# Kernel tuning notes

Measured on AMD Instinct MI355X. Metric: run time of the kernel, lower is better.

## Reference

```python
import jax, jax.numpy as jnp
import numpy as np

EPS = 1e-6      # eps used in token2map / map2token weight normalization
LN_EPS = 1e-5   # torch nn.LayerNorm default


def layernorm(x, w, b):
    m = jnp.mean(x, axis=-1, keepdims=True)
    xc = x - m
    v = jnp.mean(xc * xc, axis=-1, keepdims=True)
    return xc * jax.lax.rsqrt(v + LN_EPS) * w + b


def grid_index(H_init, W_init, H, W):
    # nearest-neighbor map: flattened feature-map index for each init-grid cell
    r = (jnp.arange(H_init) * H) // H_init
    c = (jnp.arange(W_init) * W) // W_init
    return (r[:, None] * W + c[None, :]).reshape(-1)  # [N_init]


def token2map(x, idx_token, H, W, H_init, W_init):
    # tokens [B,N,C] -> feature map [B,H,W,C] via weighted scatter-mean
    B, N, C = x.shape
    idx_hw = grid_index(H_init, W_init, H, W)                    # [N_init]
    counts = jnp.zeros((H * W,), x.dtype).at[idx_hw].add(1.0)    # identical across batch
    w = (1.0 / (counts + EPS))[idx_hw]                           # [N_init]
    src = jnp.take_along_axis(x, idx_token[..., None], axis=1)   # [B,N_init,C]
    out = jnp.zeros((B, H * W, C), x.dtype).at[:, idx_hw, :].add(src * w[None, :, None])
    return out.reshape(B, H, W, C)


def map2token(fmap, idx_token, N, H_init, W_init):
    # feature map [B,H,W,C] -> tokens [B,N,C]: mean of member grid cells per token
    B, H, W, C = fmap.shape
    idx_hw = grid_index(H_init, W_init, H, W)
    bidx = jnp.arange(B)[:, None]
    counts = jnp.zeros((B, N), fmap.dtype).at[bidx, idx_token].add(1.0)
    wt = jnp.take_along_axis(1.0 / (counts + EPS), idx_token, axis=1)  # [B,N_init]
    src = fmap.reshape(B, H * W, C)[:, idx_hw, :]                      # [B,N_init,C]
    return jnp.zeros((B, N, C), fmap.dtype).at[bidx, idx_token].add(src * wt[..., None])


def _forward(x, token_score, idx_token,
             norm1_w, norm1_b, q_w, q_b, kv_w, kv_b, sr_w, sr_b, srn_w, srn_b,
             proj_w, proj_b, norm2_w, norm2_b, fc1_w, fc1_b, skip_w, dw_w, dw_b,
             fc2_w, fc2_b, H, W, H_init, W_init, token_num, num_heads):
    B, N, C = x.shape
    d = C // num_heads
    scale = d ** -0.5
    sr = 2  # sr_ratio

    xn = layernorm(x, norm1_w, norm1_b)  # q_dict['x'] = norm1(x); kv_dict is q_dict

    # ---- TCFormerDynamicAttention ----
    q = (xn @ q_w + q_b).reshape(B, N, num_heads, d).transpose(0, 2, 1, 3)  # [B,h,N,d]
    tmp = jnp.concatenate([xn, token_score], axis=-1)            # [B,N,C+1]
    tmp_map = token2map(tmp, idx_token, H, W, H_init, W_init)    # [B,H,W,C+1]
    kv_map, conf_map = tmp_map[..., :C], tmp_map[..., C]
    kv = jax.lax.conv_general_dilated(kv_map, sr_w, (sr, sr), 'VALID',
        dimension_numbers=('NHWC', 'HWIO', 'NHWC')) + sr_b       # sr conv, stride 2
    M = (H // sr) * (W // sr)
    kv = layernorm(kv.reshape(B, M, C), srn_w, srn_b)
    conf = conf_map.reshape(B, H // sr, sr, W // sr, sr).mean(axis=(2, 4)).reshape(B, M)

    kv = (kv @ kv_w + kv_b).reshape(B, M, 2, num_heads, d)
    k = kv[:, :, 0].transpose(0, 2, 1, 3)                        # [B,h,M,d]
    v = kv[:, :, 1].transpose(0, 2, 1, 3)
    attn = jnp.einsum('bhnd,bhmd->bhnm', q * scale, k) + conf[:, None, None, :]
    attn = jax.nn.softmax(attn, axis=-1)
    a = jnp.einsum('bhnm,bhmd->bhnd', attn, v).transpose(0, 2, 1, 3).reshape(B, N, C)
    x = x + (a @ proj_w + proj_b)

    # ---- TCMLP ----
    h = layernorm(x, norm2_w, norm2_b) @ fc1_w + fc1_b           # [B,N,H1]
    hmap = token2map(h, idx_token, H, W, H_init, W_init)         # [B,H,W,H1]
    hmap = jax.lax.conv_general_dilated(hmap, dw_w, (1, 1), ((1, 1), (1, 1)),
        dimension_numbers=('NHWC', 'HWIO', 'NHWC'),
        feature_group_count=h.shape[-1]) + dw_b                  # depthwise 3x3
    hc = h * skip_w + map2token(hmap, idx_token, N, H_init, W_init)  # skip = dw 1x1 conv1d
    hc = jax.nn.gelu(hc, approximate=False)
    return x + (hc @ fc2_w + fc2_b)


def setup_inputs() -> dict:
    B, N, C, H1 = 8, 1568, 256, 1024
    H = W = 56
    H_init = W_init = 112
    key = jax.random.key(0)
    ks = jax.random.split(key, 16)
    r = lambda i, shape, s=0.02: jax.random.normal(ks[i], shape, jnp.float32) * s
    return {
        'x': jax.random.normal(ks[0], (B, N, C), jnp.float32),
        'token_score': jax.random.normal(ks[1], (B, N, 1), jnp.float32),
        'idx_token': jax.random.randint(ks[2], (B, H_init * W_init), 0, N),
        'norm1_w': jnp.ones((C,), jnp.float32), 'norm1_b': jnp.zeros((C,), jnp.float32),
        'q_w': r(3, (C, C)), 'q_b': jnp.zeros((C,), jnp.float32),
        'kv_w': r(4, (C, 2 * C)), 'kv_b': jnp.zeros((2 * C,), jnp.float32),
        'sr_w': r(5, (2, 2, C, C)), 'sr_b': jnp.zeros((C,), jnp.float32),
        'srn_w': jnp.ones((C,), jnp.float32), 'srn_b': jnp.zeros((C,), jnp.float32),
        'proj_w': r(6, (C, C)), 'proj_b': jnp.zeros((C,), jnp.float32),
        'norm2_w': jnp.ones((C,), jnp.float32), 'norm2_b': jnp.zeros((C,), jnp.float32),
        'fc1_w': r(7, (C, H1)), 'fc1_b': jnp.zeros((H1,), jnp.float32),
        'skip_w': 1.0 + r(8, (H1,), 0.1),
        'dw_w': r(9, (3, 3, 1, H1), 0.1), 'dw_b': jnp.zeros((H1,), jnp.float32),
        'fc2_w': r(10, (H1, C)), 'fc2_b': jnp.zeros((C,), jnp.float32),
        'H': H, 'W': W, 'H_init': H_init, 'W_init': W_init,
        'token_num': N, 'num_heads': 8,
    }


def reference(x, token_score, idx_token, norm1_w, norm1_b, q_w, q_b, kv_w, kv_b,
              sr_w, sr_b, srn_w, srn_b, proj_w, proj_b, norm2_w, norm2_b,
              fc1_w, fc1_b, skip_w, dw_w, dw_b, fc2_w, fc2_b,
              H, W, H_init, W_init, token_num, num_heads):
    return _forward(x, token_score, idx_token, norm1_w, norm1_b, q_w, q_b, kv_w, kv_b,
                    sr_w, sr_b, srn_w, srn_b, proj_w, proj_b, norm2_w, norm2_b,
                    fc1_w, fc1_b, skip_w, dw_w, dw_b, fc2_w, fc2_b,
                    H, W, H_init, W_init, token_num, num_heads)
```

## Files before the change

### kernel.cpp

```cpp
#include <hip/hip_runtime.h>
#include <math.h>

#define BB 8
#define NTOK 1568
#define CD 256
#define HIMG 56
#define WIMG 56
#define HWSZ 3136
#define HIG 112
#define WIG 112
#define NI 12544
#define MKV 784
#define MPAD 800
#define NHEADS 8
#define HEADD 32
#define HH1 1024
#define ROWS1 (BB*NTOK)
#define ROWSK (BB*MKV)
#define LOG2E 1.4426950408889634f

typedef unsigned short bfu;
typedef __attribute__((ext_vector_type(4))) unsigned short bf4;
typedef __attribute__((ext_vector_type(8))) unsigned short bf8;
typedef __attribute__((ext_vector_type(8))) short s8v;
typedef __attribute__((ext_vector_type(4))) float f4v;
typedef __attribute__((ext_vector_type(16))) float f16v;

__device__ inline float b2f(bfu u) { union { unsigned i; float f; } x; x.i = (unsigned)u << 16; return x.f; }
__device__ inline bfu f2b(float f) {
  union { float f; unsigned i; } x; x.f = f;
  unsigned r = x.i + 0x7fffu + ((x.i >> 16) & 1u);
  return (bfu)(r >> 16);
}
__device__ inline int get_isb(const unsigned* probe) { return probe[0] == 0x3F803F80u ? 1 : 0; }
__device__ inline float ldd(const void* p, size_t i, int isb) {
  return isb ? b2f(((const bfu*)p)[i]) : ((const float*)p)[i];
}
__device__ inline int xswz(int wg, int nwg) {
  return (nwg & 7) ? wg : (wg & 7) * (nwg >> 3) + (wg >> 3);
}

__global__ __launch_bounds__(256) void wtr_tile(const void* __restrict__ w0,
                                                const void* __restrict__ w1,
                                                const void* __restrict__ w2,
                                                const void* __restrict__ w3,
                                                const void* __restrict__ w4,
                                                const void* __restrict__ w5,
                                                const void* __restrict__ w6,
                                                const void* __restrict__ w7,
                                                bfu* __restrict__ wtb,
                                                const unsigned* __restrict__ probe) {
  int isb = get_isb(probe);
  int bid = blockIdx.x, tid = threadIdx.x;
  if (bid >= 1024) {
    int idx = (bid - 1024) * 256 + tid;
    if (idx < 9216) wtb[1048576 + idx] = f2b(ldd(w6, idx, isb));
    else            wtb[1048576 + idx] = f2b(ldd(w7, idx - 9216, isb));
    return;
  }
  const void* W; int K, N; bfu* Wt; int tloc;
  if (bid < 64)       { W = w0; K = 256;  N = 256;  Wt = wtb;          tloc = bid; }
  else if (bid < 320) { W = w1; K = 1024; N = 256;  Wt = wtb + 65536;  tloc = bid - 64; }
  else if (bid < 448) { W = w2; K = 256;  N = 512;  Wt = wtb + 327680; tloc = bid - 320; }
  else if (bid < 512) { W = w3; K = 256;  N = 256;  Wt = wtb + 458752; tloc = bid - 448; }
  else if (bid < 768) { W = w4; K = 256;  N = 1024; Wt = wtb + 524288; tloc = bid - 512; }
  else                { W = w5; K = 1024; N = 256;  Wt = wtb + 786432; tloc = bid - 768; }
  int ntn = N >> 5;
  int tn = tloc % ntn, tk = tloc / ntn;
  int n0 = tn * 32, k0 = tk * 32;
  __shared__ float s[32][33];
  int tx = tid & 31, ty = tid >> 5;
#pragma unroll
  for (int i = 0; i < 4; i++) {
    int k = ty + 8 * i;
    s[k][tx] = ldd(W, (size_t)(k0 + k) * N + n0 + tx, isb);
  }
  __syncthreads();
#pragma unroll
  for (int i = 0; i < 4; i++) {
    int n = ty + 8 * i;
    Wt[(size_t)(n0 + n) * K + k0 + tx] = f2b(s[tx][n]);
  }
}

__global__ __launch_bounds__(256) void ln_kernel(const void* __restrict__ in, int inmode,
                                                 const void* __restrict__ w,
                                                 const void* __restrict__ bta,
                                                 bfu* __restrict__ out,
                                                 const unsigned* __restrict__ probe) {
  int isb = get_isb(probe);
  int im = (inmode == 2) ? isb : inmode;
  int blk = xswz(blockIdx.x, gridDim.x);
  int wv = threadIdx.x >> 6, lane = threadIdx.x & 63;
  int row = blk * 4 + wv;
  int c4 = lane * 4;
  float v[4];
  if (im) {
    bf4 t = *(const bf4*)((const bfu*)in + (size_t)row * CD + c4);
#pragma unroll
    for (int j = 0; j < 4; j++) v[j] = b2f(t[j]);
  } else {
    float4 t = *(const float4*)((const float*)in + (size_t)row * CD + c4);
    v[0] = t.x; v[1] = t.y; v[2] = t.z; v[3] = t.w;
  }
  float s1 = v[0] + v[1] + v[2] + v[3];
  float s2 = v[0] * v[0] + v[1] * v[1] + v[2] * v[2] + v[3] * v[3];
#pragma unroll
  for (int off = 1; off < 64; off <<= 1) {
    s1 += __shfl_xor(s1, off);
    s2 += __shfl_xor(s2, off);
  }
  float m = s1 * (1.0f / CD);
  float inv = rsqrtf(s2 * (1.0f / CD) - m * m + 1e-5f);
  bf4 ov;
#pragma unroll
  for (int j = 0; j < 4; j++)
    ov[j] = f2b((v[j] - m) * inv * ldd(w, c4 + j, isb) + ldd(bta, c4 + j, isb));
  *(bf4*)(out + (size_t)row * CD + c4) = ov;
}

__global__ __launch_bounds__(256) void gemm2ph(const bfu* __restrict__ A,
                                               const bfu* __restrict__ Bt,
                                               const void* __restrict__ bias,
                                               const void* __restrict__ resid, int rmode,
                                               void* __restrict__ Cc, int cmode,
                                               void* __restrict__ aux,
                                               int K, int Ncols,
                                               const unsigned* __restrict__ probe) {
  int isb = get_isb(probe);
  int rm = (rmode == 1) ? (isb ? 3 : 2) : rmode;
  int cm = (cmode == 2) ? (isb ? 0 : 1) : cmode;
  __shared__ bfu As[2][64][40];
  __shared__ bfu Bs[2][64][40];
  int t = threadIdx.x;
  int nbx = Ncols >> 6;
  int id = xswz(blockIdx.x, gridDim.x);
  int row0 = (id / nbx) * 64, col0 = (id % nbx) * 64;
  int sr = t >> 2, sc = (t & 3) * 8;
  int w = t >> 6, lane = t & 63;
  int li = lane & 15, q = lane >> 4;
  int wm = w * 16;
  const bfu* pa = A + (size_t)(row0 + sr) * K + sc;
  const bfu* pb = Bt + (size_t)(col0 + sr) * K + sc;
  f4v zz = {0.f, 0.f, 0.f, 0.f};
  f4v acc[4];
#pragma unroll
  for (int ni = 0; ni < 4; ni++) acc[ni] = zz;
  s8v la = *(const s8v*)(pa);
  s8v lb = *(const s8v*)(pb);
  int cur = 0;
  for (int k0 = 32; k0 <= K; k0 += 32) {
    *(s8v*)(&As[cur][sr][sc]) = la;
    *(s8v*)(&Bs[cur][sr][sc]) = lb;
    __syncthreads();
    if (k0 < K) {
      la = *(const s8v*)(pa + k0);
      lb = *(const s8v*)(pb + k0);
    }
    s8v af  = *(const s8v*)(&As[cur][wm + li][q * 8]);
    s8v bf0 = *(const s8v*)(&Bs[cur][li][q * 8]);
    s8v bf1 = *(const s8v*)(&Bs[cur][16 + li][q * 8]);
    s8v bf2 = *(const s8v*)(&Bs[cur][32 + li][q * 8]);
    s8v bf3 = *(const s8v*)(&Bs[cur][48 + li][q * 8]);
    __builtin_amdgcn_s_setprio(1);
    acc[0] = __builtin_amdgcn_mfma_f32_16x16x32_bf16(af, bf0, acc[0], 0, 0, 0);
    acc[1] = __builtin_amdgcn_mfma_f32_16x16x32_bf16(af, bf1, acc[1], 0, 0, 0);
    acc[2] = __builtin_amdgcn_mfma_f32_16x16x32_bf16(af, bf2, acc[2], 0, 0, 0);
    acc[3] = __builtin_amdgcn_mfma_f32_16x16x32_bf16(af, bf3, acc[3], 0, 0, 0);
    __builtin_amdgcn_s_setprio(0);
    cur ^= 1;
  }
  float bw[4];
#pragma unroll
  for (int ni = 0; ni < 4; ni++) bw[ni] = ldd(bias, col0 + ni * 16 + li, isb);
#pragma unroll
  for (int ni = 0; ni < 4; ni++) {
    int col = col0 + ni * 16 + li;
#pragma unroll
    for (int r = 0; r < 4; r++) {
      int row = row0 + wm + q * 4 + r;
      size_t base = (size_t)row * Ncols + col;
      float v = acc[ni][r] + bw[ni];
      if (rm == 2) v += ((const float*)resid)[base];
      else if (rm == 3) v += b2f(((const bfu*)resid)[base]);
      if (cm == 0) ((bfu*)Cc)[base] = f2b(v);
      else if (cm == 1) ((float*)Cc)[base] = v;
      else {
        if (col < 256) ((bfu*)Cc)[base] = f2b(v);
        else {
          int bb = row / MKV, mm = row - bb * MKV;
          ((bfu*)aux)[((size_t)(bb * 256) + (col - 256)) * MPAD + mm] = f2b(v);
        }
      }
    }
  }
}

__global__ __launch_bounds__(256) void akv_kernel(const bfu* __restrict__ xn,
                                                  const void* __restrict__ tscore,
                                                  const int* __restrict__ idx_token,
                                                  bfu* __restrict__ Akv,
                                                  float* __restrict__ conf,
                                                  const unsigned* __restrict__ probe) {
  int isb = get_isb(probe);
  int blk = xswz(blockIdx.x, gridDim.x), tid = threadIdx.x;
  int b = blk / MKV, m = blk % MKV;
  int i2 = m / 28, j2 = m % 28;
  __shared__ int nn[16];
  __shared__ float cacc[16];
  if (tid < 16) {
    int a = (tid >> 3) & 1, kb = (tid >> 2) & 1, di = (tid >> 1) & 1, dj = tid & 1;
    int ti = 4 * i2 + 2 * a + di, tj = 4 * j2 + 2 * kb + dj;
    int n = idx_token[b * NI + ti * WIG + tj];
    nn[tid] = n;
    cacc[tid] = ldd(tscore, b * NTOK + n, isb);
  }
  __syncthreads();
  const float w4 = 1.0f / (4.0f + 1e-6f);
  int g = tid >> 6, c4 = (tid & 63) * 4;
  bf4 a0 = *(const bf4*)(xn + (size_t)(b * NTOK + nn[g * 4 + 0]) * CD + c4);
  bf4 a1 = *(const bf4*)(xn + (size_t)(b * NTOK + nn[g * 4 + 1]) * CD + c4);
  bf4 a2 = *(const bf4*)(xn + (size_t)(b * NTOK + nn[g * 4 + 2]) * CD + c4);
  bf4 a3 = *(const bf4*)(xn + (size_t)(b * NTOK + nn[g * 4 + 3]) * CD + c4);
  bf4 rv;
#pragma unroll
  for (int j = 0; j < 4; j++)
    rv[j] = f2b(w4 * (b2f(a0[j]) + b2f(a1[j]) + b2f(a2[j]) + b2f(a3[j])));
  *(bf4*)(Akv + (size_t)blk * 1024 + g * CD + c4) = rv;
  if (tid == 0) {
    float s = 0.f;
    for (int k = 0; k < 16; k++) s += cacc[k];
    conf[b * MPAD + m] = 0.25f * w4 * s * 5.656854249492381f;
  }
}

__global__ __launch_bounds__(256) void pad_kernel(bfu* __restrict__ vt, float* __restrict__ conf) {
  int t = blockIdx.x * 256 + threadIdx.x;
  int b = t / 4096, rem = t % 4096;
  int d = rem / 16, m = MKV + (rem % 16);
  vt[((size_t)(b * 256 + d)) * MPAD + m] = 0;
  if (t < 128) conf[(t / 16) * MPAD + MKV + (t % 16)] = -1e30f;
}

__global__ __launch_bounds__(256) void attn_kernel(const bfu* __restrict__ qb,
                                                   const bfu* __restrict__ kv,
                                                   const bfu* __restrict__ vt,
                                                   const float* __restrict__ conf,
                                                   bfu* __restrict__ out) {
  __shared__ float sdata[4][64][34];
  int tid = threadIdx.x;
  int w = tid >> 6, lane = tid & 63;
  int l31 = lane & 31, hi = lane >> 5;
  int blk = xswz(blockIdx.x, gridDim.x);
  int qt = blk % 25, tt = blk / 25;
  int hh = tt & 7, b = tt >> 3;
  int n0 = qt * 64;
  int two = (qt < 24);
  const bfu* qrow1 = qb + (size_t)(b * NTOK + n0 + l31) * CD + hh * HEADD + hi * 8;
  s8v qfA1 = *(const s8v*)(qrow1);
  s8v qfB1 = *(const s8v*)(qrow1 + 16);
  s8v qfA2 = {0, 0, 0, 0, 0, 0, 0, 0}, qfB2 = qfA2;
  if (two) {
    const bfu* qrow2 = qrow1 + (size_t)32 * CD;
    qfA2 = *(const s8v*)(qrow2);
    qfB2 = *(const s8v*)(qrow2 + 16);
  }
  const float scale = 0.17677669529663689f * LOG2E;
  const bfu* kbase = kv + hh * HEADD + hi * 8;
  const bfu* vbase = vt + ((size_t)(b * 256 + hh * HEADD + l31)) * MPAD + hi * 8;
  const float* cbase = conf + b * MPAD + 4 * hi;
  f16v oc1, oc2;
#pragma unroll
  for (int r = 0; r < 16; r++) { oc1[r] = 0.f; oc2[r] = 0.f; }
  float lr1 = 0.f, lr2 = 0.f;
  int w32 = w * 32;
  const bfu* kp0 = kbase + (size_t)(b * MKV + w32 + l31) * 512;
  s8v kfA = *(const s8v*)(kp0);
  s8v kfB = *(const s8v*)(kp0 + 16);
  s8v vfA = *(const s8v*)(vbase + w32);
  s8v vfB = *(const s8v*)(vbase + w32 + 16);
  float4 cf0 = *(const float4*)(cbase + w32);
  float4 cf1 = *(const float4*)(cbase + w32 + 8);
  float4 cf2 = *(const float4*)(cbase + w32 + 16);
  float4 cf3 = *(const float4*)(cbase + w32 + 24);
  for (int m0 = w32; m0 < MPAD; m0 += 128) {
    s8v ckA = kfA, ckB = kfB, cvA = vfA, cvB = vfB;
    float4 d0 = cf0, d1 = cf1, d2 = cf2, d3 = cf3;
    int m1 = m0 + 128;
    if (m1 < MPAD) {
      int mA = m1 + l31; if (mA > MKV - 1) mA = MKV - 1;
      const bfu* kp = kbase + (size_t)(b * MKV + mA) * 512;
      kfA = *(const s8v*)(kp);
      kfB = *(const s8v*)(kp + 16);
      vfA = *(const s8v*)(vbase + m1);
      vfB = *(const s8v*)(vbase + m1 + 16);
      cf0 = *(const float4*)(cbase + m1);
      cf1 = *(const float4*)(cbase + m1 + 8);
      cf2 = *(const float4*)(cbase + m1 + 16);
      cf3 = *(const float4*)(cbase + m1 + 24);
    }
    f16v cseed;
    cseed[0] = d0.x; cseed[1] = d0.y; cseed[2] = d0.z; cseed[3] = d0.w;
    cseed[4] = d1.x; cseed[5] = d1.y; cseed[6] = d1.z; cseed[7] = d1.w;
    cseed[8] = d2.x; cseed[9] = d2.y; cseed[10] = d2.z; cseed[11] = d2.w;
    cseed[12] = d3.x; cseed[13] = d3.y; cseed[14] = d3.z; cseed[15] = d3.w;
    __builtin_amdgcn_s_setprio(1);
    f16v c = __builtin_amdgcn_mfma_f32_32x32x16_bf16(ckA, qfA1, cseed, 0, 0, 0);
    c = __builtin_amdgcn_mfma_f32_32x32x16_bf16(ckB, qfB1, c, 0, 0, 0);
    __builtin_amdgcn_s_setprio(0);
    {
      float p[16], ps0 = 0.f, ps1 = 0.f, ps2 = 0.f, ps3 = 0.f;
#pragma unroll
      for (int r = 0; r < 16; r++) {
        p[r] = __builtin_amdgcn_exp2f(c[r] * scale);
        if ((r & 3) == 0) ps0 += p[r];
        else if ((r & 3) == 1) ps1 += p[r];
        else if ((r & 3) == 2) ps2 += p[r];
        else ps3 += p[r];
      }
      lr1 += (ps0 + ps1) + (ps2 + ps3);
      unsigned Z[8];
#pragma unroll
      for (int a2 = 0; a2 < 8; a2++)
        asm("v_cvt_pk_bf16_f32 %0, %1, %2" : "=v"(Z[a2]) : "v"(p[2 * a2]), "v"(p[2 * a2 + 1]));
      asm("v_permlane32_swap_b32 %0, %1" : "+v"(Z[0]), "+v"(Z[2]));
      asm("v_permlane32_swap_b32 %0, %1" : "+v"(Z[1]), "+v"(Z[3]));
      asm("v_permlane32_swap_b32 %0, %1" : "+v"(Z[4]), "+v"(Z[6]));
      asm("v_permlane32_swap_b32 %0, %1" : "+v"(Z[5]), "+v"(Z[7]));
      union { unsigned u[4]; s8v v; } B1, B2;
      B1.u[0] = Z[0]; B1.u[1] = Z[1]; B1.u[2] = Z[2]; B1.u[3] = Z[3];
      B2.u[0] = Z[4]; B2.u[1] = Z[5]; B2.u[2] = Z[6]; B2.u[3] = Z[7];
      __builtin_amdgcn_s_setprio(1);
      oc1 = __builtin_amdgcn_mfma_f32_32x32x16_bf16(cvA, B1.v, oc1, 0, 0, 0);
      oc1 = __builtin_amdgcn_mfma_f32_32x32x16_bf16(cvB, B2.v, oc1, 0, 0, 0);
      __builtin_amdgcn_s_setprio(0);
    }
    if (two) {
      __builtin_amdgcn_s_setprio(1);
      f16v c2 = __builtin_amdgcn_mfma_f32_32x32x16_bf16(ckA, qfA2, cseed, 0, 0, 0);
      c2 = __builtin_amdgcn_mfma_f32_32x32x16_bf16(ckB, qfB2, c2, 0, 0, 0);
      __builtin_amdgcn_s_setprio(0);
      float p[16], ps0 = 0.f, ps1 = 0.f, ps2 = 0.f, ps3 = 0.f;
#pragma unroll
      for (int r = 0; r < 16; r++) {
        p[r] = __builtin_amdgcn_exp2f(c2[r] * scale);
        if ((r & 3) == 0) ps0 += p[r];
        else if ((r & 3) == 1) ps1 += p[r];
        else if ((r & 3) == 2) ps2 += p[r];
        else ps3 += p[r];
      }
      lr2 += (ps0 + ps1) + (ps2 + ps3);
      unsigned Z[8];
#pragma unroll
      for (int a2 = 0; a2 < 8; a2++)
        asm("v_cvt_pk_bf16_f32 %0, %1, %2" : "=v"(Z[a2]) : "v"(p[2 * a2]), "v"(p[2 * a2 + 1]));
      asm("v_permlane32_swap_b32 %0, %1" : "+v"(Z[0]), "+v"(Z[2]));
      asm("v_permlane32_swap_b32 %0, %1" : "+v"(Z[1]), "+v"(Z[3]));
      asm("v_permlane32_swap_b32 %0, %1" : "+v"(Z[4]), "+v"(Z[6]));
      asm("v_permlane32_swap_b32 %0, %1" : "+v"(Z[5]), "+v"(Z[7]));
      union { unsigned u[4]; s8v v; } B1, B2;
      B1.u[0] = Z[0]; B1.u[1] = Z[1]; B1.u[2] = Z[2]; B1.u[3] = Z[3];
      B2.u[0] = Z[4]; B2.u[1] = Z[5]; B2.u[2] = Z[6]; B2.u[3] = Z[7];
      __builtin_amdgcn_s_setprio(1);
      oc2 = __builtin_amdgcn_mfma_f32_32x32x16_bf16(cvA, B1.v, oc2, 0, 0, 0);
      oc2 = __builtin_amdgcn_mfma_f32_32x32x16_bf16(cvB, B2.v, oc2, 0, 0, 0);
      __builtin_amdgcn_s_setprio(0);
    }
  }
#pragma unroll
  for (int r = 0; r < 16; r++) { sdata[w][lane][r] = oc1[r]; sdata[w][lane][17 + r] = oc2[r]; }
  sdata[w][lane][16] = lr1;
  sdata[w][lane][33] = lr2;
  __syncthreads();
  if (w == 0 || (w == 1 && two)) {
    int base = w * 17;
    float s[17];
#pragma unroll
    for (int r = 0; r < 17; r++)
      s[r] = sdata[0][lane][base + r] + sdata[1][lane][base + r] +
             sdata[2][lane][base + r] + sdata[3][lane][base + r];
    float l = s[16];
    l += __shfl_xor(l, 32);
    float inv = 1.0f / l;
    bfu* op = out + (size_t)(b * NTOK + n0 + w * 32 + l31) * CD + hh * HEADD + 4 * hi;
#pragma unroll
    for (int g = 0; g < 4; g++) {
      bf4 o;
#pragma unroll
      for (int u = 0; u < 4; u++) o[u] = f2b(s[4 * g + u] * inv);
      *(bf4*)(op + 8 * g) = o;
    }
  }
}

__global__ __launch_bounds__(128) void hmap_kernel(const bfu* __restrict__ h,
                                                   const int* __restrict__ idx_token,
                                                   bfu* __restrict__ hmap) {
  int blk = xswz(blockIdx.x, gridDim.x), tid = threadIdx.x;
  int b = blk / HWSZ, cell = blk % HWSZ;
  int i = cell / WIMG, j = cell % WIMG;
  __shared__ int nn[4];
  if (tid < 4) {
    int di = tid >> 1, dj = tid & 1;
    nn[tid] = idx_token[b * NI + (2 * i + di) * WIG + (2 * j + dj)];
  }
  __syncthreads();
  const float w4 = 1.0f / (4.0f + 1e-6f);
  int c8 = tid * 8;
  bf8 a0 = *(const bf8*)(h + (size_t)(b * NTOK + nn[0]) * HH1 + c8);
  bf8 a1 = *(const bf8*)(h + (size_t)(b * NTOK + nn[1]) * HH1 + c8);
  bf8 a2 = *(const bf8*)(h + (size_t)(b * NTOK + nn[2]) * HH1 + c8);
  bf8 a3 = *(const bf8*)(h + (size_t)(b * NTOK + nn[3]) * HH1 + c8);
  bf8 rv;
#pragma unroll
  for (int j2 = 0; j2 < 8; j2++)
    rv[j2] = f2b(w4 * (b2f(a0[j2]) + b2f(a1[j2]) + b2f(a2[j2]) + b2f(a3[j2])));
  *(bf8*)(hmap + (size_t)blk * HH1 + c8) = rv;
}

__global__ __launch_bounds__(256) void dw_kernel(const bfu* __restrict__ hmap,
                                                 const bfu* __restrict__ dwt,
                                                 const bfu* __restrict__ dbt,
                                                 bfu* __restrict__ dwout) {
  int blk = xswz(blockIdx.x, gridDim.x);
  int j4 = blk % 14; int rem = blk / 14;
  int i = rem % HIMG; int b = rem / HIMG;
  int tid = threadIdx.x;
  int c4 = tid * 4;
  int j0 = j4 * 4;
  float wf[9][4];
#pragma unroll
  for (int k = 0; k < 9; k++) {
    bf4 wv = *(const bf4*)(dwt + k * HH1 + c4);
#pragma unroll
    for (int u = 0; u < 4; u++) wf[k][u] = b2f(wv[u]);
  }
  bf4 bias = *(const bf4*)(dbt + c4);
  float bi[4];
#pragma unroll
  for (int u = 0; u < 4; u++) bi[u] = b2f(bias[u]);
  bf4 tp[3][6];
  const size_t bbase = (size_t)b * HWSZ;
#pragma unroll
  for (int r = 0; r < 3; r++) {
    int yy = i - 1 + r;
    bool rowok = (unsigned)yy < (unsigned)HIMG;
#pragma unroll
    for (int cc = 0; cc < 6; cc++) {
      int xx = j0 - 1 + cc;
      bf4 v = {0, 0, 0, 0};
      if (rowok && (unsigned)xx < (unsigned)WIMG)
        v = *(const bf4*)(hmap + (bbase + yy * WIMG + xx) * HH1 + c4);
      tp[r][cc] = v;
    }
  }
#pragma unroll
  for (int j = 0; j < 4; j++) {
    float acc[4] = {bi[0], bi[1], bi[2], bi[3]};
#pragma unroll
    for (int r = 0; r < 3; r++)
#pragma unroll
      for (int kx = 0; kx < 3; kx++) {
        bf4 hv = tp[r][j + kx];
#pragma unroll
        for (int u = 0; u < 4; u++) acc[u] += b2f(hv[u]) * wf[r * 3 + kx][u];
      }
    bf4 ov;
#pragma unroll
    for (int u = 0; u < 4; u++) ov[u] = f2b(acc[u]);
    *(bf4*)(dwout + (bbase + i * WIMG + j0 + j) * HH1 + c4) = ov;
  }
}

__global__ void zero_int(int* p) { p[blockIdx.x * 256 + threadIdx.x] = 0; }
__global__ void count_kernel(const int* __restrict__ idx, int* __restrict__ cnt) {
  int t = xswz(blockIdx.x, gridDim.x) * 256 + threadIdx.x;
  int b = t / NI;
  atomicAdd(&cnt[b * NTOK + idx[t]], 1);
}
__global__ __launch_bounds__(256) void scan_kernel(const int* __restrict__ cnt, int* __restrict__ offs) {
  int b = blockIdx.x, tid = threadIdx.x;
  __shared__ int s[NTOK];
  for (int i = tid; i < NTOK; i += 256) s[i] = cnt[b * NTOK + i];
  __syncthreads();
  for (int st = 1; st < NTOK; st <<= 1) {
    int vals[7]; int k = 0;
    for (int i = tid; i < NTOK; i += 256, k++) vals[k] = (i >= st) ? s[i - st] : 0;
    __syncthreads();
    k = 0;
    for (int i = tid; i < NTOK; i += 256, k++) s[i] += vals[k];
    __syncthreads();
  }
  for (int i = tid; i < NTOK; i += 256) offs[b * NTOK + i] = (i > 0) ? s[i - 1] : 0;
}
__global__ void fill_kernel(const int* __restrict__ idx, const int* __restrict__ offs,
                            int* __restrict__ cursor, int* __restrict__ tlist) {
  int t = xswz(blockIdx.x, gridDim.x) * 256 + threadIdx.x;
  int b = t / NI, tt = t % NI;
  int n = idx[t];
  int p = atomicAdd(&cursor[b * NTOK + n], 1);
  tlist[b * NI + offs[b * NTOK + n] + p] = tt;
}

__global__ __launch_bounds__(128) void m2t_kernel(const bfu* __restrict__ h,
                                                  const bfu* __restrict__ dwout,
                                                  const int* __restrict__ cnt,
                                                  const int* __restrict__ offs,
                                                  const int* __restrict__ tlist,
                                                  const void* __restrict__ skipw,
                                                  bfu* __restrict__ hc,
                                                  const unsigned* __restrict__ probe) {
  int isb = get_isb(probe);
  int blk = xswz(blockIdx.x, gridDim.x), tid = threadIdx.x;
  int b = blk / NTOK, n = blk % NTOK;
  int c = cnt[b * NTOK + n];
  int o0 = offs[b * NTOK + n];
  float inv = 1.0f / ((float)c + 1e-6f);
  int c8 = tid * 8;
  float a[8] = {};
  for (int k = 0; k < c; k++) {
    int tt = tlist[b * NI + o0 + k];
    int ti = tt / WIG, tj = tt % WIG;
    int cell = (ti >> 1) * WIMG + (tj >> 1);
    bf8 dv = *(const bf8*)(dwout + ((size_t)b * HWSZ + cell) * HH1 + c8);
#pragma unroll
    for (int j2 = 0; j2 < 8; j2++) a[j2] += b2f(dv[j2]);
  }
  bf8 hv = *(const bf8*)(h + (size_t)blk * HH1 + c8);
  bf8 ov;
  const float is2 = 0.70710678118654752f;
#pragma unroll
  for (int j2 = 0; j2 < 8; j2++) {
    float r = b2f(hv[j2]) * ldd(skipw, c8 + j2, isb) + a[j2] * inv;
    r = 0.5f * r * (1.0f + erff(r * is2));
    ov[j2] = f2b(r);
  }
  *(bf8*)(hc + (size_t)blk * HH1 + c8) = ov;
}

extern "C" void kernel_launch(void* const* d_in, const int* in_sizes, int n_in,
                              void* d_out, int out_size, void* d_ws, size_t ws_size,
                              hipStream_t stream) {
  const void* x        = d_in[0];
  const void* tscore   = d_in[1];
  const int*  idx_tok  = (const int*)d_in[2];
  const void* norm1_w  = d_in[3];
  const void* norm1_b  = d_in[4];
  const void* q_w      = d_in[5];
  const void* q_b      = d_in[6];
  const void* kv_w     = d_in[7];
  const void* kv_b     = d_in[8];
  const void* sr_w     = d_in[9];
  const void* sr_b     = d_in[10];
  const void* srn_w    = d_in[11];
  const void* srn_b    = d_in[12];
  const void* proj_w   = d_in[13];
  const void* proj_b   = d_in[14];
  const void* norm2_w  = d_in[15];
  const void* norm2_b  = d_in[16];
  const void* fc1_w    = d_in[17];
  const void* fc1_b    = d_in[18];
  const void* skip_w   = d_in[19];
  const void* dw_w     = d_in[20];
  const void* dw_b     = d_in[21];
  const void* fc2_w    = d_in[22];
  const void* fc2_b    = d_in[23];
  const unsigned* probe = (const unsigned*)d_in[3];

  float* ws = (float*)d_ws;
  size_t o = 0;
  float* x2 = ws + o;          o += (size_t)ROWS1 * CD;
  float* hR = ws + o;          o += (size_t)ROWS1 * HH1 / 2;
  float* mR = ws + o;          o += (size_t)BB * HWSZ * HH1 / 2;
  float* dR = ws + o;          o += (size_t)BB * HWSZ * HH1 / 2;
  int* ibase = (int*)(ws + o); o += (size_t)(3 * ROWS1 + BB * NI);
  bfu* wtb   = (bfu*)(ws + o); o += 529408;
  bfu* vtb   = (bfu*)(ws + o);

  bfu* Akv   = (bfu*)hR;
  bfu* kvc   = (bfu*)(hR + (size_t)ROWSK * 1024 / 2);
  bfu* h     = (bfu*)hR;
  bfu* qbuf  = (bfu*)mR;
  bfu* kvout = (bfu*)(mR + (size_t)ROWS1 * CD / 2);
  float* conf  = mR + (size_t)ROWS1 * CD / 2 + (size_t)ROWSK * 512 / 2;
  bfu* hmap  = (bfu*)mR;
  bfu* hc    = (bfu*)mR;
  bfu* xn    = (bfu*)dR;
  bfu* dwout = (bfu*)dR;
  int* counts = ibase;
  int* cursor = ibase + ROWS1;
  int* offs   = ibase + 2 * ROWS1;
  int* tlist  = ibase + 3 * ROWS1;
  bfu* q_wt    = wtb;
  bfu* sr_wt   = wtb + 65536;
  bfu* kv_wt   = wtb + 327680;
  bfu* proj_wt = wtb + 458752;
  bfu* fc1_wt  = wtb + 524288;
  bfu* fc2_wt  = wtb + 786432;
  bfu* dwt     = wtb + 1048576;
  bfu* dbt     = wtb + 1057792;

  wtr_tile<<<1064, 256, 0, stream>>>(q_w, sr_w, kv_w, proj_w, fc1_w, fc2_w, dw_w, dw_b, wtb, probe);
  pad_kernel<<<128, 256, 0, stream>>>(vtb, conf);

  ln_kernel<<<ROWS1 / 4, 256, 0, stream>>>(x, 2, norm1_w, norm1_b, xn, probe);
  gemm2ph<<<784, 256, 0, stream>>>(xn, q_wt, q_b, nullptr, 0, qbuf, 0, nullptr, 256, 256, probe);
  akv_kernel<<<ROWSK, 256, 0, stream>>>(xn, tscore, idx_tok, Akv, conf, probe);
  gemm2ph<<<392, 256, 0, stream>>>(Akv, sr_wt, sr_b, nullptr, 0, kvc, 0, nullptr, 1024, 256, probe);
  ln_kernel<<<ROWSK / 4, 256, 0, stream>>>(kvc, 1, srn_w, srn_b, kvc, probe);
  gemm2ph<<<784, 256, 0, stream>>>(kvc, kv_wt, kv_b, nullptr, 0, kvout, 3, vtb, 256, 512, probe);
  attn_kernel<<<BB * NHEADS * 25, 256, 0, stream>>>(qbuf, kvout, vtb, conf, xn);
  gemm2ph<<<784, 256, 0, stream>>>(xn, proj_wt, proj_b, x, 1, x2, 1, nullptr, 256, 256, probe);
  ln_kernel<<<ROWS1 / 4, 256, 0, stream>>>(x2, 0, norm2_w, norm2_b, xn, probe);
  gemm2ph<<<3136, 256, 0, stream>>>(xn, fc1_wt, fc1_b, nullptr, 0, h, 0, nullptr, 256, 1024, probe);
  hmap_kernel<<<BB * HWSZ, 128, 0, stream>>>(h, idx_tok, hmap);
  dw_kernel<<<BB * HIMG * 14, 256, 0, stream>>>(hmap, dwt, dbt, dwout);
  zero_int<<<(2 * ROWS1) / 256, 256, 0, stream>>>(counts);
  count_kernel<<<(BB * NI) / 256, 256, 0, stream>>>(idx_tok, counts);
  scan_kernel<<<BB, 256, 0, stream>>>(counts, offs);
  fill_kernel<<<(BB * NI) / 256, 256, 0, stream>>>(idx_tok, offs, cursor, tlist);
  m2t_kernel<<<ROWS1, 128, 0, stream>>>(h, dwout, counts, offs, tlist, skip_w, hc, probe);
  gemm2ph<<<784, 256, 0, stream>>>(hc, fc2_wt, fc2_b, x2, 2, d_out, 2, nullptr, 1024, 256, probe);
}
```

Measured before the change: 408.5 us.

## Fold pad into weight-transpose, memset counts, halve attn LDS, batch tlist loads

Merges the padding kernel into the weight transpose launch and replaces the zero_int kernel with an async memset issued early, which removes launches. The attention epilogue now reduces the two 32-row halves one after the other, so the shared buffer is half the size, at the cost of extra barriers. The m2t kernel loads up to 8 tlist entries per lane and broadcasts them with shuffles, which replaces serial dependent index loads.

```diff
diff --git a/kernel.cpp b/kernel.cpp
--- a/kernel.cpp
+++ b/kernel.cpp
@@ -49,9 +49,19 @@
                                                 const void* __restrict__ w6,
                                                 const void* __restrict__ w7,
                                                 bfu* __restrict__ wtb,
+                                                bfu* __restrict__ vt,
+                                                float* __restrict__ conf,
                                                 const unsigned* __restrict__ probe) {
   int isb = get_isb(probe);
   int bid = blockIdx.x, tid = threadIdx.x;
+  if (bid >= 1064) {
+    int t = (bid - 1064) * 256 + tid;
+    int b = t / 4096, rem = t % 4096;
+    int d = rem / 16, m = MKV + (rem % 16);
+    vt[((size_t)(b * 256 + d)) * MPAD + m] = 0;
+    if (t < 128) conf[(t / 16) * MPAD + MKV + (t % 16)] = -1e30f;
+    return;
+  }
   if (bid >= 1024) {
     int idx = (bid - 1024) * 256 + tid;
     if (idx < 9216) wtb[1048576 + idx] = f2b(ldd(w6, idx, isb));
@@ -234,20 +244,12 @@
   }
 }
 
-__global__ __launch_bounds__(256) void pad_kernel(bfu* __restrict__ vt, float* __restrict__ conf) {
-  int t = blockIdx.x * 256 + threadIdx.x;
-  int b = t / 4096, rem = t % 4096;
-  int d = rem / 16, m = MKV + (rem % 16);
-  vt[((size_t)(b * 256 + d)) * MPAD + m] = 0;
-  if (t < 128) conf[(t / 16) * MPAD + MKV + (t % 16)] = -1e30f;
-}
-
 __global__ __launch_bounds__(256) void attn_kernel(const bfu* __restrict__ qb,
                                                    const bfu* __restrict__ kv,
                                                    const bfu* __restrict__ vt,
                                                    const float* __restrict__ conf,
                                                    bfu* __restrict__ out) {
-  __shared__ float sdata[4][64][34];
+  __shared__ float sdata[4][64][17];
   int tid = threadIdx.x;
   int w = tid >> 6, lane = tid & 63;
   int l31 = lane & 31, hi = lane >> 5;
@@ -368,27 +370,48 @@
     }
   }
 #pragma unroll
-  for (int r = 0; r < 16; r++) { sdata[w][lane][r] = oc1[r]; sdata[w][lane][17 + r] = oc2[r]; }
+  for (int r = 0; r < 16; r++) sdata[w][lane][r] = oc1[r];
   sdata[w][lane][16] = lr1;
-  sdata[w][lane][33] = lr2;
   __syncthreads();
-  if (w == 0 || (w == 1 && two)) {
-    int base = w * 17;
+  if (w == 0) {
     float s[17];
 #pragma unroll
     for (int r = 0; r < 17; r++)
-      s[r] = sdata[0][lane][base + r] + sdata[1][lane][base + r] +
-             sdata[2][lane][base + r] + sdata[3][lane][base + r];
+      s[r] = sdata[0][lane][r] + sdata[1][lane][r] + sdata[2][lane][r] + sdata[3][lane][r];
     float l = s[16];
     l += __shfl_xor(l, 32);
     float inv = 1.0f / l;
-    bfu* op = out + (size_t)(b * NTOK + n0 + w * 32 + l31) * CD + hh * HEADD + 4 * hi;
+    bfu* op = out + (size_t)(b * NTOK + n0 + l31) * CD + hh * HEADD + 4 * hi;
 #pragma unroll
     for (int g = 0; g < 4; g++) {
       bf4 o;
 #pragma unroll
       for (int u = 0; u < 4; u++) o[u] = f2b(s[4 * g + u] * inv);
       *(bf4*)(op + 8 * g) = o;
+    }
+  }
+  if (two) {
+    __syncthreads();
+#pragma unroll
+    for (int r = 0; r < 16; r++) sdata[w][lane][r] = oc2[r];
+    sdata[w][lane][16] = lr2;
+    __syncthreads();
+    if (w == 0) {
+      float s[17];
+#pragma unroll
+      for (int r = 0; r < 17; r++)
+        s[r] = sdata[0][lane][r] + sdata[1][lane][r] + sdata[2][lane][r] + sdata[3][lane][r];
+      float l = s[16];
+      l += __shfl_xor(l, 32);
+      float inv = 1.0f / l;
+      bfu* op = out + (size_t)(b * NTOK + n0 + 32 + l31) * CD + hh * HEADD + 4 * hi;
+#pragma unroll
+      for (int g = 0; g < 4; g++) {
+        bf4 o;
+#pragma unroll
+        for (int u = 0; u < 4; u++) o[u] = f2b(s[4 * g + u] * inv);
+        *(bf4*)(op + 8 * g) = o;
+      }
     }
   }
 }
@@ -472,7 +495,6 @@
   }
 }
 
-__global__ void zero_int(int* p) { p[blockIdx.x * 256 + threadIdx.x] = 0; }
 __global__ void count_kernel(const int* __restrict__ idx, int* __restrict__ cnt) {
   int t = xswz(blockIdx.x, gridDim.x) * 256 + threadIdx.x;
   int b = t / NI;
@@ -512,19 +534,28 @@
                                                   const unsigned* __restrict__ probe) {
   int isb = get_isb(probe);
   int blk = xswz(blockIdx.x, gridDim.x), tid = threadIdx.x;
+  int lane = tid & 63;
   int b = blk / NTOK, n = blk % NTOK;
   int c = cnt[b * NTOK + n];
   int o0 = offs[b * NTOK + n];
   float inv = 1.0f / ((float)c + 1e-6f);
   int c8 = tid * 8;
   float a[8] = {};
-  for (int k = 0; k < c; k++) {
-    int tt = tlist[b * NI + o0 + k];
-    int ti = tt / WIG, tj = tt % WIG;
-    int cell = (ti >> 1) * WIMG + (tj >> 1);
-    bf8 dv = *(const bf8*)(dwout + ((size_t)b * HWSZ + cell) * HH1 + c8);
-#pragma unroll
-    for (int j2 = 0; j2 < 8; j2++) a[j2] += b2f(dv[j2]);
+  for (int k0 = 0; k0 < c; k0 += 8) {
+    int kk = k0 + (lane & 7);
+    int e = 0;
+    if (kk < c) e = tlist[b * NI + o0 + kk];
+#pragma unroll
+    for (int j = 0; j < 8; j++) {
+      if (k0 + j < c) {
+        int tt = __shfl(e, j);
+        int ti = tt / WIG, tj = tt % WIG;
+        int cell = (ti >> 1) * WIMG + (tj >> 1);
+        bf8 dv = *(const bf8*)(dwout + ((size_t)b * HWSZ + cell) * HH1 + c8);
+#pragma unroll
+        for (int j2 = 0; j2 < 8; j2++) a[j2] += b2f(dv[j2]);
+      }
+    }
   }
   bf8 hv = *(const bf8*)(h + (size_t)blk * HH1 + c8);
   bf8 ov;
@@ -600,8 +631,9 @@
   bfu* dwt     = wtb + 1048576;
   bfu* dbt     = wtb + 1057792;
 
-  wtr_tile<<<1064, 256, 0, stream>>>(q_w, sr_w, kv_w, proj_w, fc1_w, fc2_w, dw_w, dw_b, wtb, probe);
-  pad_kernel<<<128, 256, 0, stream>>>(vtb, conf);
+  wtr_tile<<<1192, 256, 0, stream>>>(q_w, sr_w, kv_w, proj_w, fc1_w, fc2_w, dw_w, dw_b,
+                                     wtb, vtb, conf, probe);
+  hipMemsetAsync(counts, 0, (size_t)(2 * ROWS1) * sizeof(int), stream);
 
   ln_kernel<<<ROWS1 / 4, 256, 0, stream>>>(x, 2, norm1_w, norm1_b, xn, probe);
   gemm2ph<<<784, 256, 0, stream>>>(xn, q_wt, q_b, nullptr, 0, qbuf, 0, nullptr, 256, 256, probe);
@@ -615,7 +647,6 @@
   gemm2ph<<<3136, 256, 0, stream>>>(xn, fc1_wt, fc1_b, nullptr, 0, h, 0, nullptr, 256, 1024, probe);
   hmap_kernel<<<BB * HWSZ, 128, 0, stream>>>(h, idx_tok, hmap);
   dw_kernel<<<BB * HIMG * 14, 256, 0, stream>>>(hmap, dwt, dbt, dwout);
-  zero_int<<<(2 * ROWS1) / 256, 256, 0, stream>>>(counts);
   count_kernel<<<(BB * NI) / 256, 256, 0, stream>>>(idx_tok, counts);
   scan_kernel<<<BB, 256, 0, stream>>>(counts, offs);
   fill_kernel<<<(BB * NI) / 256, 256, 0, stream>>>(idx_tok, offs, cursor, tlist);
```

Result: no change. 404.9 us (-0.9%).
